# Performance work log

Hardware: AMD Instinct MI355X
Metric: run time of the kernel (lower is better)

## Reference

```python
import jax, jax.numpy as jnp
import numpy as np

C = 384
K = 13
EPS = 1e-5

def bn(y, g, b, m, v):
    # inference-mode BatchNorm2d over channel dim of NCHW
    scale = (g / jnp.sqrt(v + EPS)).reshape(1, -1, 1, 1)
    shift = (b - m * g / jnp.sqrt(v + EPS)).reshape(1, -1, 1, 1)
    return y * scale + shift

def dwconv(x, w):
    # depthwise KxK conv, SAME padding, w: [C,1,K,K]
    p = w.shape[-1] // 2
    return jax.lax.conv_general_dilated(
        x, w, window_strides=(1, 1), padding=[(p, p), (p, p)],
        dimension_numbers=('NCHW', 'OIHW', 'NCHW'),
        feature_group_count=x.shape[1])

def setup_inputs() -> dict:
    key = jax.random.key(0)
    ks = jax.random.split(key, 16)
    f32 = jnp.float32
    inp = {
        'x':     jax.random.normal(ks[0], (16, C, 56, 56), dtype=f32),
        'pw_w':  jax.random.normal(ks[1], (C, C), dtype=f32) * 0.05,
        'pw_g':  jax.random.uniform(ks[2], (C,), dtype=f32) + 0.5,
        'pw_b':  jax.random.normal(ks[3], (C,), dtype=f32) * 0.1,
        'pw_m':  jax.random.normal(ks[4], (C,), dtype=f32) * 0.1,
        'pw_v':  jax.random.uniform(ks[5], (C,), dtype=f32) + 0.5,
        'dwk_w': jax.random.normal(ks[6], (C, 1, K, K), dtype=f32) * 0.05,
        'dwk_g': jax.random.uniform(ks[7], (C,), dtype=f32) + 0.5,
        'dwk_b': jax.random.normal(ks[8], (C,), dtype=f32) * 0.1,
        'dwk_m': jax.random.normal(ks[9], (C,), dtype=f32) * 0.1,
        'dwk_v': jax.random.uniform(ks[10], (C,), dtype=f32) + 0.5,
        'dw1_w': jax.random.normal(ks[11], (C,), dtype=f32) * 0.5,
        'dw1_g': jax.random.uniform(ks[12], (C,), dtype=f32) + 0.5,
        'dw1_b': jax.random.normal(ks[13], (C,), dtype=f32) * 0.1,
        'dw1_m': jax.random.normal(ks[14], (C,), dtype=f32) * 0.1,
        'dw1_v': jax.random.uniform(ks[15], (C,), dtype=f32) + 0.5,
    }
    return inp

def reference(x, pw_w, pw_g, pw_b, pw_m, pw_v,
              dwk_w, dwk_g, dwk_b, dwk_m, dwk_v,
              dw1_w, dw1_g, dw1_b, dw1_m, dw1_v):
    # pointwise conv (1x1, dense over channels) + BN, residual add
    y = jnp.einsum('bchw,oc->bohw', x, pw_w)
    x_pw = bn(y, pw_g, pw_b, pw_m, pw_v) + x
    # large-kernel depthwise branch
    out = bn(dwconv(x_pw, dwk_w), dwk_g, dwk_b, dwk_m, dwk_v)
    # 1x1 depthwise branch = per-channel scale
    out = out + bn(x_pw * dw1_w.reshape(1, -1, 1, 1), dw1_g, dw1_b, dw1_m, dw1_v)
    return jax.nn.gelu(out, approximate=False)
```

## Files before the change

kernel.cpp:

```cpp
#include <hip/hip_runtime.h>

#define CC 384
#define HW 3136
#define WIDTH 56
#define PLANE_ELEMS (CC*HW)
#define EPS 1e-5f

#define SLOT_U 6272
#define HALF_U 3136

#define WROW 40
#define WSTEP_U (CC*WROW)
#define WP_TOTAL (12*WSTEP_U)

#define BT_U 6656
#define BT_TOTAL (CC*BT_U)

typedef __attribute__((ext_vector_type(8))) short bf16x8;
typedef __attribute__((ext_vector_type(4))) float f32x4;

static __device__ __forceinline__ float bf2f(unsigned short u) {
  union { unsigned int i; float f; } x; x.i = ((unsigned int)u) << 16; return x.f;
}
static __device__ __forceinline__ unsigned short f2bf(float f) {
  union { float f; unsigned int i; } x; x.f = f;
  unsigned int r = x.i + 0x7fffu + ((x.i >> 16) & 1u);
  return (unsigned short)(r >> 16);
}

__global__ __launch_bounds__(256) void pack_w(
    const float* __restrict__ wmat, unsigned short* __restrict__ wp)
{
  int i = blockIdx.x * 256 + threadIdx.x;
  int kt  = i / WSTEP_U;
  int rem = i - kt * WSTEP_U;
  int o   = rem / WROW;
  int kk  = rem - o * WROW;
  unsigned short v = 0;
  if (kk < 32) v = f2bf(wmat[o * CC + kt * 32 + kk]);
  wp[i] = v;
}

__global__ __launch_bounds__(256) void pack_bt(
    const float* __restrict__ dwkw, unsigned short* __restrict__ btg)
{
  const int c = blockIdx.x;
  for (int i = threadIdx.x; i < BT_U; i += 256) {
    int ky = i >> 9, rem = i & 511, n = rem >> 5, k = rem & 31;
    int kx = k - n - 2;
    unsigned short v = 0;
    if ((unsigned)kx < 13u) v = f2bf(dwkw[c * 169 + ky * 13 + kx]);
    btg[(size_t)c * BT_U + i] = v;
  }
}

__global__ __launch_bounds__(256, 3) void pw_gemm_bn_res(
    const float* __restrict__ xin,
    const unsigned short* __restrict__ wp,
    const float* __restrict__ pwg, const float* __restrict__ pwb,
    const float* __restrict__ pwm, const float* __restrict__ pwv,
    unsigned short* __restrict__ xpw)
{
  __shared__ __align__(16) unsigned short Xt[64 * 40];
  __shared__ __align__(16) unsigned short Wt[WSTEP_U];
  __shared__ float scaleS[CC];
  __shared__ float shiftS[CC];

  const int tid = threadIdx.x;
  const int j0 = blockIdx.x * 64;
  const int b  = blockIdx.y;
  const size_t bbase = (size_t)b * PLANE_ELEMS;

  for (int o = tid; o < CC; o += 256) {
    float s = pwg[o] * rsqrtf(pwv[o] + EPS);
    scaleS[o] = s;
    shiftS[o] = pwb[o] - pwm[o] * s;
  }

  const int lane = tid & 63;
  const int wid  = tid >> 6;
  const int l15  = lane & 15;
  const int q    = lane >> 4;

  f32x4 acc[4][6] = {};

  const float* xsrc0 = xin + bbase + (size_t)(wid * 8) * HW + (j0 + lane);

  for (int kt = 0; kt < 12; ++kt) {
    const int c0 = kt * 32;
    __syncthreads();
    {
      const float* src = xsrc0 + (size_t)c0 * HW;
      float v0 = src[0 * HW], v1 = src[1 * HW], v2 = src[2 * HW], v3 = src[3 * HW];
      float v4 = src[4 * HW], v5 = src[5 * HW], v6 = src[6 * HW], v7 = src[7 * HW];
      bf16x8 u;
      u[0] = (short)f2bf(v0); u[1] = (short)f2bf(v1);
      u[2] = (short)f2bf(v2); u[3] = (short)f2bf(v3);
      u[4] = (short)f2bf(v4); u[5] = (short)f2bf(v5);
      u[6] = (short)f2bf(v6); u[7] = (short)f2bf(v7);
      *((bf16x8*)&Xt[lane * 40 + wid * 8]) = u;
    }
    {
      const unsigned short* g = wp + (size_t)kt * WSTEP_U;
      #pragma unroll
      for (int i = 0; i < 8; ++i) {
        int c = i * 4 + wid;
        if (c < 30) {
          __builtin_amdgcn_global_load_lds(
              (const __attribute__((address_space(1))) unsigned int*)(g + c * 512 + lane * 8),
              (__attribute__((address_space(3))) unsigned int*)(&Wt[c * 512]),
              16, 0, 0);
        }
      }
    }
    __syncthreads();

    bf16x8 a[4];
    #pragma unroll
    for (int jf = 0; jf < 4; ++jf)
      a[jf] = *((const bf16x8*)&Xt[(jf * 16 + l15) * 40 + q * 8]);

    #pragma unroll
    for (int of = 0; of < 6; ++of) {
      bf16x8 bb = *((const bf16x8*)&Wt[(wid * 96 + of * 16 + l15) * WROW + q * 8]);
      #pragma unroll
      for (int jf = 0; jf < 4; ++jf)
        acc[jf][of] = __builtin_amdgcn_mfma_f32_16x16x32_bf16(a[jf], bb, acc[jf][of], 0, 0, 0);
    }
  }

  const int ob = wid * 96;
  #pragma unroll
  for (int of = 0; of < 6; ++of) {
    const int o = ob + of * 16 + l15;
    const float s = scaleS[o], t = shiftS[o];
    #pragma unroll
    for (int jf = 0; jf < 4; ++jf) {
      const int j = j0 + jf * 16 + q * 4;
      f32x4 av = acc[jf][of];
      float4 xr = *((const float4*)(xin + bbase + (size_t)o * HW + j));
      ushort4 w4;
      w4.x = f2bf(av[0] * s + t + xr.x);
      w4.y = f2bf(av[1] * s + t + xr.y);
      w4.z = f2bf(av[2] * s + t + xr.z);
      w4.w = f2bf(av[3] * s + t + xr.w);
      size_t pidx = (size_t)(b * CC + o) * SLOT_U + HALF_U + j;
      *((ushort4*)(xpw + pidx)) = w4;
    }
  }
}

#define TSTRIDE 88
#define TROWS 76
#define NCH 11

__global__ __launch_bounds__(256) void dw_conv_mfma(
    float* __restrict__ outf,
    const unsigned short* __restrict__ stash,
    const unsigned short* __restrict__ btg,
    const float* __restrict__ dwkw,
    const float* __restrict__ dkg, const float* __restrict__ dkb,
    const float* __restrict__ dkm, const float* __restrict__ dkv,
    const float* __restrict__ d1w,
    const float* __restrict__ d1g, const float* __restrict__ d1b,
    const float* __restrict__ d1m, const float* __restrict__ d1v)
{
  __shared__ __align__(16) unsigned short tile[TROWS * TSTRIDE];
  __shared__ __align__(16) unsigned short Bt[13 * 16 * 32];

  const int bc = blockIdx.x;
  const int c = bc % CC;
  const size_t plane_u = (size_t)bc * SLOT_U + HALF_U;
  const size_t plane_f = (size_t)bc * HW;
  const int tid = threadIdx.x;
  const int lane = tid & 63;
  const int wid  = tid >> 6;

  for (int i = tid; i < TROWS * NCH; i += 256) {
    int r = i / NCH, ch = i - r * NCH;
    int gy = r - 6;
    bf16x8 v = {0,0,0,0,0,0,0,0};
    if ((unsigned)gy < (unsigned)WIDTH && ch >= 1 && ch <= 7)
      v = *((const bf16x8*)(stash + plane_u + gy * WIDTH + (ch - 1) * 8));
    *((bf16x8*)&tile[r * TSTRIDE + ch * 8]) = v;
  }

  if (btg) {
    const unsigned short* g = btg + (size_t)c * BT_U;
    #pragma unroll
    for (int i = 0; i < 4; ++i) {
      int ch = i * 4 + wid;
      if (ch < 13) {
        __builtin_amdgcn_global_load_lds(
            (const __attribute__((address_space(1))) unsigned int*)(g + ch * 512 + lane * 8),
            (__attribute__((address_space(3))) unsigned int*)(&Bt[ch * 512]),
            16, 0, 0);
      }
    }
  } else {
    for (int i = tid; i < 13 * 512; i += 256) {
      int ky = i >> 9, rem = i & 511, n = rem >> 5, k = rem & 31;
      int kx = k - n - 2;
      float wv = ((unsigned)kx < 13u) ? dwkw[c * 169 + ky * 13 + kx] : 0.f;
      Bt[i] = f2bf(wv);
    }
  }

  const float sk = dkg[c] * rsqrtf(dkv[c] + EPS);
  const float tk = dkb[c] - dkm[c] * sk;
  const float s1 = d1g[c] * rsqrtf(d1v[c] + EPS);
  const float a1 = d1w[c] * s1;
  const float t1 = d1b[c] - d1m[c] * s1;
  const float tsum = tk + t1;

  __syncthreads();

  const int l15  = lane & 15;
  const int q    = lane >> 4;

  bf16x8 bfr[13];
  #pragma unroll
  for (int ky = 0; ky < 13; ++ky)
    bfr[ky] = *((const bf16x8*)&Bt[(ky * 16 + l15) * 32 + q * 8]);

  for (int t = wid; t < 16; t += 4) {
    const int y0 = (t >> 2) * 16, x0 = (t & 3) * 16;
    f32x4 acc = {0.f, 0.f, 0.f, 0.f};
    #pragma unroll
    for (int ky = 0; ky < 13; ++ky) {
      bf16x8 a = *((const bf16x8*)&tile[(y0 + l15 + ky) * TSTRIDE + x0 + q * 8]);
      acc = __builtin_amdgcn_mfma_f32_16x16x32_bf16(a, bfr[ky], acc, 0, 0, 0);
    }
    const int x = x0 + l15;
    if (x < WIDTH) {
      #pragma unroll
      for (int r = 0; r < 4; ++r) {
        const int y = y0 + q * 4 + r;
        if (y < WIDTH) {
          float ctr = bf2f(tile[(y + 6) * TSTRIDE + x + 8]);
          float v = acc[r] * sk + tsum + ctr * a1;
          outf[plane_f + y * WIDTH + x] =
              0.5f * v * (1.f + erff(v * 0.70710678118654752f));
        }
      }
    }
  }
}

extern "C" void kernel_launch(void* const* d_in, const int* in_sizes, int n_in,
                              void* d_out, int out_size, void* d_ws, size_t ws_size,
                              hipStream_t stream) {
  const float* x     = (const float*)d_in[0];
  const float* pw_w  = (const float*)d_in[1];
  const float* pw_g  = (const float*)d_in[2];
  const float* pw_b  = (const float*)d_in[3];
  const float* pw_m  = (const float*)d_in[4];
  const float* pw_v  = (const float*)d_in[5];
  const float* dwk_w = (const float*)d_in[6];
  const float* dwk_g = (const float*)d_in[7];
  const float* dwk_b = (const float*)d_in[8];
  const float* dwk_m = (const float*)d_in[9];
  const float* dwk_v = (const float*)d_in[10];
  const float* dw1_w = (const float*)d_in[11];
  const float* dw1_g = (const float*)d_in[12];
  const float* dw1_b = (const float*)d_in[13];
  const float* dw1_m = (const float*)d_in[14];
  const float* dw1_v = (const float*)d_in[15];
  float* outf = (float*)d_out;
  unsigned short* outu = (unsigned short*)d_out;
  unsigned short* wpack = (unsigned short*)d_ws;

  pack_w<<<WP_TOTAL / 256, 256, 0, stream>>>(pw_w, wpack);

  unsigned short* btg = nullptr;
  if (ws_size >= (size_t)(WP_TOTAL + BT_TOTAL) * sizeof(unsigned short)) {
    btg = wpack + WP_TOTAL;
    pack_bt<<<CC, 256, 0, stream>>>(dwk_w, btg);
  }

  dim3 gridA(HW / 64, 16);
  pw_gemm_bn_res<<<gridA, 256, 0, stream>>>(x, wpack, pw_g, pw_b, pw_m, pw_v, outu);

  dim3 gridB(16 * CC);
  dw_conv_mfma<<<gridB, 256, 0, stream>>>(outf, outu, btg, dwk_w,
      dwk_g, dwk_b, dwk_m, dwk_v, dw1_w, dw1_g, dw1_b, dw1_m, dw1_v);
}
```

Measured before the change: 255.4 us.

## Split pointwise GEMM output channels across grid and prefetch X into registers

```diff
diff --git a/kernel.cpp b/kernel.cpp
--- a/kernel.cpp
+++ b/kernel.cpp
@@ -15,6 +15,9 @@
 
 #define BT_U 6656
 #define BT_TOTAL (CC*BT_U)
+
+#define OHALF 192
+#define WHALF_U (OHALF*WROW)
 
 typedef __attribute__((ext_vector_type(8))) short bf16x8;
 typedef __attribute__((ext_vector_type(4))) float f32x4;
@@ -54,7 +57,7 @@
   }
 }
 
-__global__ __launch_bounds__(256, 3) void pw_gemm_bn_res(
+__global__ __launch_bounds__(256, 5) void pw_gemm_bn_res(
     const float* __restrict__ xin,
     const unsigned short* __restrict__ wp,
     const float* __restrict__ pwg, const float* __restrict__ pwb,
@@ -62,19 +65,21 @@
     unsigned short* __restrict__ xpw)
 {
   __shared__ __align__(16) unsigned short Xt[64 * 40];
-  __shared__ __align__(16) unsigned short Wt[WSTEP_U];
-  __shared__ float scaleS[CC];
-  __shared__ float shiftS[CC];
+  __shared__ __align__(16) unsigned short Wt[WHALF_U];
+  __shared__ float scaleS[OHALF];
+  __shared__ float shiftS[OHALF];
 
   const int tid = threadIdx.x;
   const int j0 = blockIdx.x * 64;
-  const int b  = blockIdx.y;
+  const int o0 = blockIdx.y * OHALF;
+  const int b  = blockIdx.z;
   const size_t bbase = (size_t)b * PLANE_ELEMS;
 
-  for (int o = tid; o < CC; o += 256) {
+  if (tid < OHALF) {
+    int o = o0 + tid;
     float s = pwg[o] * rsqrtf(pwv[o] + EPS);
-    scaleS[o] = s;
-    shiftS[o] = pwb[o] - pwm[o] * s;
+    scaleS[tid] = s;
+    shiftS[tid] = pwb[o] - pwm[o] * s;
   }
 
   const int lane = tid & 63;
@@ -82,30 +87,28 @@
   const int l15  = lane & 15;
   const int q    = lane >> 4;
 
-  f32x4 acc[4][6] = {};
+  f32x4 acc[4][3] = {};
 
   const float* xsrc0 = xin + bbase + (size_t)(wid * 8) * HW + (j0 + lane);
 
+  float xv[8];
+  #pragma unroll
+  for (int i = 0; i < 8; ++i) xv[i] = xsrc0[(size_t)i * HW];
+
   for (int kt = 0; kt < 12; ++kt) {
-    const int c0 = kt * 32;
     __syncthreads();
     {
-      const float* src = xsrc0 + (size_t)c0 * HW;
-      float v0 = src[0 * HW], v1 = src[1 * HW], v2 = src[2 * HW], v3 = src[3 * HW];
-      float v4 = src[4 * HW], v5 = src[5 * HW], v6 = src[6 * HW], v7 = src[7 * HW];
       bf16x8 u;
-      u[0] = (short)f2bf(v0); u[1] = (short)f2bf(v1);
-      u[2] = (short)f2bf(v2); u[3] = (short)f2bf(v3);
-      u[4] = (short)f2bf(v4); u[5] = (short)f2bf(v5);
-      u[6] = (short)f2bf(v6); u[7] = (short)f2bf(v7);
+      #pragma unroll
+      for (int i = 0; i < 8; ++i) u[i] = (short)f2bf(xv[i]);
       *((bf16x8*)&Xt[lane * 40 + wid * 8]) = u;
     }
     {
-      const unsigned short* g = wp + (size_t)kt * WSTEP_U;
-      #pragma unroll
-      for (int i = 0; i < 8; ++i) {
+      const unsigned short* g = wp + (size_t)kt * WSTEP_U + (size_t)o0 * WROW;
+      #pragma unroll
+      for (int i = 0; i < 4; ++i) {
         int c = i * 4 + wid;
-        if (c < 30) {
+        if (c < 15) {
           __builtin_amdgcn_global_load_lds(
               (const __attribute__((address_space(1))) unsigned int*)(g + c * 512 + lane * 8),
               (__attribute__((address_space(3))) unsigned int*)(&Wt[c * 512]),
@@ -113,6 +116,11 @@
         }
       }
     }
+    if (kt < 11) {
+      const float* src = xsrc0 + (size_t)(kt + 1) * 32 * HW;
+      #pragma unroll
+      for (int i = 0; i < 8; ++i) xv[i] = src[(size_t)i * HW];
+    }
     __syncthreads();
 
     bf16x8 a[4];
@@ -121,19 +129,20 @@
       a[jf] = *((const bf16x8*)&Xt[(jf * 16 + l15) * 40 + q * 8]);
 
     #pragma unroll
-    for (int of = 0; of < 6; ++of) {
-      bf16x8 bb = *((const bf16x8*)&Wt[(wid * 96 + of * 16 + l15) * WROW + q * 8]);
+    for (int of = 0; of < 3; ++of) {
+      bf16x8 bb = *((const bf16x8*)&Wt[(wid * 48 + of * 16 + l15) * WROW + q * 8]);
       #pragma unroll
       for (int jf = 0; jf < 4; ++jf)
         acc[jf][of] = __builtin_amdgcn_mfma_f32_16x16x32_bf16(a[jf], bb, acc[jf][of], 0, 0, 0);
     }
   }
 
-  const int ob = wid * 96;
+  const int ob = wid * 48;
   #pragma unroll
-  for (int of = 0; of < 6; ++of) {
-    const int o = ob + of * 16 + l15;
-    const float s = scaleS[o], t = shiftS[o];
+  for (int of = 0; of < 3; ++of) {
+    const int oo = ob + of * 16 + l15;
+    const int o = o0 + oo;
+    const float s = scaleS[oo], t = shiftS[oo];
     #pragma unroll
     for (int jf = 0; jf < 4; ++jf) {
       const int j = j0 + jf * 16 + q * 4;
@@ -278,7 +287,7 @@
     pack_bt<<<CC, 256, 0, stream>>>(dwk_w, btg);
   }
 
-  dim3 gridA(HW / 64, 16);
+  dim3 gridA(HW / 64, 2, 16);
   pw_gemm_bn_res<<<gridA, 256, 0, stream>>>(x, wpack, pw_g, pw_b, pw_m, pw_v, outu);
 
   dim3 gridB(16 * CC);
```

Measured after the change: 268.9 us. 5.3% more time.

## Pre-stage X and W into MFMA fragment layout and split GEMM over outputs

Applied to the files above, without the earlier changes.

```diff
diff --git a/kernel.cpp b/kernel.cpp
--- a/kernel.cpp
+++ b/kernel.cpp
@@ -9,12 +9,15 @@
 #define SLOT_U 6272
 #define HALF_U 3136
 
+#define WF_U (12*24*64*8)
+#define BT_U 6656
+#define BT_TOTAL (CC*BT_U)
+#define XF_U (16*49*12*4*64*8)
+#define WS_FAST_BYTES ((size_t)(WF_U + BT_TOTAL + XF_U) * 2)
+
 #define WROW 40
 #define WSTEP_U (CC*WROW)
 #define WP_TOTAL (12*WSTEP_U)
-
-#define BT_U 6656
-#define BT_TOTAL (CC*BT_U)
 
 typedef __attribute__((ext_vector_type(8))) short bf16x8;
 typedef __attribute__((ext_vector_type(4))) float f32x4;
@@ -28,7 +31,115 @@
   return (unsigned short)(r >> 16);
 }
 
-__global__ __launch_bounds__(256) void pack_w(
+__global__ __launch_bounds__(256) void pack_wf(
+    const float* __restrict__ wmat, unsigned short* __restrict__ wf)
+{
+  int t = blockIdx.x * 256 + threadIdx.x;
+  int kt  = t / (24 * 64);
+  int rem = t - kt * 24 * 64;
+  int og  = rem >> 6;
+  int lane = rem & 63;
+  int o  = og * 16 + (lane & 15);
+  int k0 = kt * 32 + (lane >> 4) * 8;
+  bf16x8 u;
+  #pragma unroll
+  for (int i = 0; i < 8; ++i) u[i] = (short)f2bf(wmat[o * CC + k0 + i]);
+  *((bf16x8*)(wf + (size_t)t * 8)) = u;
+}
+
+__global__ __launch_bounds__(256) void pack_bt(
+    const float* __restrict__ dwkw, unsigned short* __restrict__ btg)
+{
+  const int c = blockIdx.x;
+  for (int i = threadIdx.x; i < BT_U; i += 256) {
+    int ky = i >> 9, rem = i & 511, n = rem >> 5, k = rem & 31;
+    int kx = k - n - 2;
+    unsigned short v = 0;
+    if ((unsigned)kx < 13u) v = f2bf(dwkw[c * 169 + ky * 13 + kx]);
+    btg[(size_t)c * BT_U + i] = v;
+  }
+}
+
+__global__ __launch_bounds__(256) void stage_xfrag(
+    const float* __restrict__ xin, unsigned short* __restrict__ xf)
+{
+  __shared__ __align__(16) unsigned short Xt[64 * 40];
+  const int kt = blockIdx.x, jt = blockIdx.y, b = blockIdx.z;
+  const int tid = threadIdx.x;
+  const int lane = tid & 63, wid = tid >> 6;
+  const int l15 = lane & 15, q = lane >> 4;
+
+  const float* src = xin + (size_t)b * PLANE_ELEMS
+                   + (size_t)(kt * 32 + wid * 8) * HW + jt * 64 + lane;
+  bf16x8 u;
+  #pragma unroll
+  for (int i = 0; i < 8; ++i) u[i] = (short)f2bf(src[(size_t)i * HW]);
+  *((bf16x8*)&Xt[lane * 40 + wid * 8]) = u;
+  __syncthreads();
+  bf16x8 f = *((const bf16x8*)&Xt[(wid * 16 + l15) * 40 + q * 8]);
+  *((bf16x8*)(xf + ((size_t)((b * 49 + jt) * 12 + kt) * 4 + wid) * 512
+                 + lane * 8)) = f;
+}
+
+__global__ __launch_bounds__(256, 3) void pw_gemm_frag(
+    const float* __restrict__ xin,
+    const unsigned short* __restrict__ wf,
+    const unsigned short* __restrict__ xf,
+    const float* __restrict__ pwg, const float* __restrict__ pwb,
+    const float* __restrict__ pwm, const float* __restrict__ pwv,
+    unsigned short* __restrict__ xpw)
+{
+  const int tid = threadIdx.x;
+  const int jt = blockIdx.x, oh = blockIdx.y, b = blockIdx.z;
+  const int j0 = jt * 64;
+  const int lane = tid & 63, wid = tid >> 6;
+  const int l15 = lane & 15, q = lane >> 4;
+  const size_t bbase = (size_t)b * PLANE_ELEMS;
+
+  f32x4 acc[4][3] = {};
+
+  const unsigned short* xbase = xf + (size_t)(b * 49 + jt) * (12 * 2048) + lane * 8;
+  const unsigned short* wbase = wf + lane * 8;
+  const int ogb = oh * 12 + wid * 3;
+
+  #pragma unroll 2
+  for (int kt = 0; kt < 12; ++kt) {
+    bf16x8 a[4];
+    #pragma unroll
+    for (int jf = 0; jf < 4; ++jf)
+      a[jf] = *((const bf16x8*)(xbase + (kt * 4 + jf) * 512));
+    #pragma unroll
+    for (int of = 0; of < 3; ++of) {
+      bf16x8 w = *((const bf16x8*)(wbase + (kt * 24 + ogb + of) * 512));
+      #pragma unroll
+      for (int jf = 0; jf < 4; ++jf)
+        acc[jf][of] = __builtin_amdgcn_mfma_f32_16x16x32_bf16(a[jf], w, acc[jf][of], 0, 0, 0);
+    }
+  }
+
+  const int o0 = oh * 192 + wid * 48;
+  #pragma unroll
+  for (int of = 0; of < 3; ++of) {
+    const int o = o0 + of * 16 + l15;
+    const float s = pwg[o] * rsqrtf(pwv[o] + EPS);
+    const float t = pwb[o] - pwm[o] * s;
+    #pragma unroll
+    for (int jf = 0; jf < 4; ++jf) {
+      const int j = j0 + jf * 16 + q * 4;
+      f32x4 av = acc[jf][of];
+      float4 xr = *((const float4*)(xin + bbase + (size_t)o * HW + j));
+      ushort4 w4;
+      w4.x = f2bf(av[0] * s + t + xr.x);
+      w4.y = f2bf(av[1] * s + t + xr.y);
+      w4.z = f2bf(av[2] * s + t + xr.z);
+      w4.w = f2bf(av[3] * s + t + xr.w);
+      size_t pidx = (size_t)(b * CC + o) * SLOT_U + HALF_U + j;
+      *((ushort4*)(xpw + pidx)) = w4;
+    }
+  }
+}
+
+__global__ __launch_bounds__(256) void pack_w_old(
     const float* __restrict__ wmat, unsigned short* __restrict__ wp)
 {
   int i = blockIdx.x * 256 + threadIdx.x;
@@ -41,20 +152,7 @@
   wp[i] = v;
 }
 
-__global__ __launch_bounds__(256) void pack_bt(
-    const float* __restrict__ dwkw, unsigned short* __restrict__ btg)
-{
-  const int c = blockIdx.x;
-  for (int i = threadIdx.x; i < BT_U; i += 256) {
-    int ky = i >> 9, rem = i & 511, n = rem >> 5, k = rem & 31;
-    int kx = k - n - 2;
-    unsigned short v = 0;
-    if ((unsigned)kx < 13u) v = f2bf(dwkw[c * 169 + ky * 13 + kx]);
-    btg[(size_t)c * BT_U + i] = v;
-  }
-}
-
-__global__ __launch_bounds__(256, 3) void pw_gemm_bn_res(
+__global__ __launch_bounds__(256, 3) void pw_gemm_bn_res_old(
     const float* __restrict__ xin,
     const unsigned short* __restrict__ wp,
     const float* __restrict__ pwg, const float* __restrict__ pwb,
@@ -83,7 +181,6 @@
   const int q    = lane >> 4;
 
   f32x4 acc[4][6] = {};
-
   const float* xsrc0 = xin + bbase + (size_t)(wid * 8) * HW + (j0 + lane);
 
   for (int kt = 0; kt < 12; ++kt) {
@@ -268,18 +365,33 @@
   const float* dw1_v = (const float*)d_in[15];
   float* outf = (float*)d_out;
   unsigned short* outu = (unsigned short*)d_out;
-  unsigned short* wpack = (unsigned short*)d_ws;
-
-  pack_w<<<WP_TOTAL / 256, 256, 0, stream>>>(pw_w, wpack);
+  unsigned short* ws = (unsigned short*)d_ws;
 
   unsigned short* btg = nullptr;
-  if (ws_size >= (size_t)(WP_TOTAL + BT_TOTAL) * sizeof(unsigned short)) {
-    btg = wpack + WP_TOTAL;
+
+  if (ws_size >= WS_FAST_BYTES) {
+    unsigned short* wf = ws;
+    btg               = ws + WF_U;
+    unsigned short* xf = ws + WF_U + BT_TOTAL;
+
+    pack_wf<<<(12*24*64)/256, 256, 0, stream>>>(pw_w, wf);
     pack_bt<<<CC, 256, 0, stream>>>(dwk_w, btg);
-  }
-
-  dim3 gridA(HW / 64, 16);
-  pw_gemm_bn_res<<<gridA, 256, 0, stream>>>(x, wpack, pw_g, pw_b, pw_m, pw_v, outu);
+
+    dim3 gridT(12, 49, 16);
+    stage_xfrag<<<gridT, 256, 0, stream>>>(x, xf);
+
+    dim3 gridA(49, 2, 16);
+    pw_gemm_frag<<<gridA, 256, 0, stream>>>(x, wf, xf, pw_g, pw_b, pw_m, pw_v, outu);
+  } else {
+    unsigned short* wpack = ws;
+    pack_w_old<<<WP_TOTAL / 256, 256, 0, stream>>>(pw_w, wpack);
+    if (ws_size >= (size_t)(WP_TOTAL + BT_TOTAL) * sizeof(unsigned short)) {
+      btg = wpack + WP_TOTAL;
+      pack_bt<<<CC, 256, 0, stream>>>(dwk_w, btg);
+    }
+    dim3 gridA(HW / 64, 16);
+    pw_gemm_bn_res_old<<<gridA, 256, 0, stream>>>(x, wpack, pw_g, pw_b, pw_m, pw_v, outu);
+  }
 
   dim3 gridB(16 * CC);
   dw_conv_mfma<<<gridB, 256, 0, stream>>>(outf, outu, btg, dwk_w,
```

Measured after the change: 254.4 us. No clear change (-0.4%).
